# Optimization experiments

Measured on AMD Instinct MI355X. Metric: run time of the kernel, lower is better.

Reference implementation:

```python
import jax, jax.numpy as jnp
import numpy as np

N = 100000   # nodes
E = 1600000  # edges
IN, HID, CLS = 128, 64, 32


def gcn_conv(x, src, dst, W, b, num_nodes):
    """PyG-style GCNConv: out = D^{-1/2} (A+I) D^{-1/2} X W + b."""
    xw = x @ W  # transform first (matches PyG: propagate on transformed feats)
    loop = jnp.arange(num_nodes)
    src_f = jnp.concatenate([src, loop])
    dst_f = jnp.concatenate([dst, loop])
    ones = jnp.ones(src_f.shape[0], dtype=xw.dtype)
    deg = jax.ops.segment_sum(ones, dst_f, num_segments=num_nodes)
    dinv = jnp.where(deg > 0, jax.lax.rsqrt(deg), 0.0)
    norm = dinv[src_f] * dinv[dst_f]            # [E+N]
    msg = xw[src_f] * norm[:, None]             # gather + scale
    out = jax.ops.segment_sum(msg, dst_f, num_segments=num_nodes)
    return out + b


def setup_inputs() -> dict:
    key = jax.random.key(0)
    k = jax.random.split(key, 7)
    x = jax.random.normal(k[0], (N, IN), dtype=jnp.float32)
    edge_index = jax.random.randint(k[1], (2, E), 0, N)
    edge_attr = jax.random.normal(k[2], (E, 1), dtype=jnp.float32)
    W1 = jax.random.normal(k[3], (IN, HID), dtype=jnp.float32) / np.sqrt(IN)
    b1 = jnp.zeros((HID,), dtype=jnp.float32)
    W2 = jax.random.normal(k[4], (HID, CLS), dtype=jnp.float32) / np.sqrt(HID)
    b2 = jnp.zeros((CLS,), dtype=jnp.float32)
    return {"x": x, "edge_index": edge_index, "edge_attr": edge_attr,
            "W1": W1, "b1": b1, "W2": W2, "b2": b2}


def reference(x, edge_index, edge_attr, W1, b1, W2, b2):
    # edge_attr is unpacked by the original forward but unused by GCNConv
    src, dst = edge_index[0], edge_index[1]
    h = jax.nn.relu(gcn_conv(x, src, dst, W1, b1, N))
    return gcn_conv(h, src, dst, W2, b2, N)
```

## Files before the change

### kernel.cpp

```cpp
#include <hip/hip_runtime.h>
#include <hip/hip_fp16.h>

#define N_NODES 100000
#define N_EDGES 1600000
#define IN_F 128
#define HID_F 64
#define CLS_F 32

#define NBKT 512
#define BKT_NODES 196
#define NBLK 800
#define EPB 2000
#define CAPB_RAW 4096
#define CAPB 5120
#define XW_BLOCKS 1563

typedef short s8v __attribute__((ext_vector_type(8)));
typedef float f4v __attribute__((ext_vector_type(4)));
typedef _Float16 h2v __attribute__((ext_vector_type(2)));

__device__ __forceinline__ unsigned short f2h(float f) {
    return __half_as_ushort(__float2half_rn(f));
}
__device__ __forceinline__ int packh2(float x, float y) {
    __half2 p = __floats2half2_rn(x, y);
    union { __half2 h; int i; } c; c.h = p; return c.i;
}

__device__ __forceinline__ void mix8(float* a, int4 v, float dv) {
    union { int4 i; __half h[8]; } c; c.i = v;
#pragma unroll
    for (int j = 0; j < 8; j++)
        a[j] = fmaf(__half2float(c.h[j]), dv, a[j]);
}

__device__ __forceinline__ void dot4(float* a, int2 v) {
#if __has_builtin(__builtin_amdgcn_fdot2)
    union { int2 i; h2v h[2]; } c; c.i = v;
    const h2v E0 = {(_Float16)1.f, (_Float16)0.f};
    const h2v E1 = {(_Float16)0.f, (_Float16)1.f};
#pragma unroll
    for (int j = 0; j < 2; j++) {
        a[2 * j]     = __builtin_amdgcn_fdot2(c.h[j], E0, a[2 * j], false);
        a[2 * j + 1] = __builtin_amdgcn_fdot2(c.h[j], E1, a[2 * j + 1], false);
    }
#else
    union { int2 i; __half2 h[2]; } c; c.i = v;
#pragma unroll
    for (int j = 0; j < 2; j++) {
        float2 f = __half22float2(c.h[j]);
        a[2 * j] += f.x; a[2 * j + 1] += f.y;
    }
#endif
}


__global__ __launch_bounds__(256) void bucket_scatter_kernel(
        const int* __restrict__ src, const int* __restrict__ dst,
        int* __restrict__ cursor, unsigned* __restrict__ bkt) {
    __shared__ int h[NBKT];
    __shared__ int base[NBKT];
    __shared__ int lcur[NBKT];
    __shared__ unsigned pkS[EPB];
    __shared__ short gS[EPB];
    int t = threadIdx.x;
    for (int i = t; i < NBKT; i += 256) { h[i] = 0; lcur[i] = 0; }
    __syncthreads();

    int e0 = blockIdx.x * EPB;
    for (int i = t; i < EPB; i += 256) {
        int e = e0 + i;
        int d = dst[e];
        int g = d / BKT_NODES;
        pkS[i] = ((unsigned)(d - g * BKT_NODES) << 17) | (unsigned)src[e];
        gS[i] = (short)g;
        atomicAdd(&h[g], 1);
    }
    __syncthreads();

    for (int g = t; g < NBKT; g += 256)
        if (h[g] > 0) base[g] = g * CAPB_RAW + atomicAdd(&cursor[g], h[g]);
    __syncthreads();

    for (int i = t; i < EPB; i += 256) {
        int g = gS[i];
        int p = base[g] + atomicAdd(&lcur[g], 1);
        bkt[p] = pkS[i];
    }
}

#define XBM 64
#define SMEM_BYTES 33792

__device__ __forceinline__ void sort_body(char* smem, int b,
        const int* __restrict__ cursor, const unsigned* __restrict__ bkt,
        int* __restrict__ csr, int* __restrict__ off, int* __restrict__ endp,
        float* __restrict__ dinv) {
    int* hist  = (int*)smem;
    int* loff  = hist + BKT_NODES;
    int* loffB = loff + BKT_NODES;
    int* wt    = loffB + BKT_NODES;
    int* csrS  = wt + 4;
    int t = threadIdx.x;
    int s0 = b * CAPB_RAW;
    int nE = cursor[b];

    for (int i = t; i < BKT_NODES; i += 256) hist[i] = 0;
    __syncthreads();
    for (int i = t; i < nE; i += 256)
        atomicAdd(&hist[bkt[s0 + i] >> 17], 1);
    __syncthreads();

    int h0 = 0, h1 = 0;
    if (t < 98) { h0 = hist[2 * t]; h1 = hist[2 * t + 1]; }
    int p0 = (h0 + 7) & ~7;
    int p1 = (h1 + 7) & ~7;
    int sum = p0 + p1;
    int lane = t & 63, w = t >> 6;
    int s = sum;
#pragma unroll
    for (int d = 1; d < 64; d <<= 1) {
        int u = __shfl_up(s, d);
        if (lane >= d) s += u;
    }
    if (lane == 63) wt[w] = s;
    __syncthreads();
    int wbase = 0;
    for (int i = 0; i < w; i++) wbase += wt[i];
    int excl = wbase + s - sum;
    if (t < 98) {
        loff[2 * t] = excl;         loffB[2 * t] = excl;
        loff[2 * t + 1] = excl + p0; loffB[2 * t + 1] = excl + p0;
    }
    __syncthreads();

    for (int j = t; j < BKT_NODES; j += 256) {
        int n = b * BKT_NODES + j;
        if (n < N_NODES) {
            int c = hist[j];
            int o = b * CAPB + loff[j];
            off[n] = o;
            endp[n] = o + ((c + 7) & ~7);
            dinv[n] = rsqrtf((float)(c + 1));
        }
    }
    __syncthreads();

    for (int i = t; i < nE; i += 256) {
        unsigned pk = bkt[s0 + i];
        int dl = (int)(pk >> 17);
        int p = atomicAdd(&loff[dl], 1);
        csrS[p] = (int)(pk & 0x1FFFFu);
    }
    __syncthreads();

    for (int j = t; j < BKT_NODES; j += 256) {
        int c = hist[j];
        int bse = loffB[j];
        int pe = bse + ((c + 7) & ~7);
        for (int p = bse + c; p < pe; p++) csrS[p] = N_NODES;
    }
    __syncthreads();

    int padTot = wt[0] + wt[1] + wt[2] + wt[3];
    for (int i = t; i < padTot; i += 256) csr[b * CAPB + i] = csrS[i];
}

__device__ __forceinline__ void xw1_body(char* smem, int xb_id,
        const float* __restrict__ x, const float* __restrict__ W1,
        unsigned short* __restrict__ y1h) {
    unsigned short* Wb = (unsigned short*)smem;
    unsigned short (*xbuf)[IN_F + 8] =
        (unsigned short (*)[IN_F + 8])(smem + 16384);
    int tid = threadIdx.x;

    for (int i = tid; i < IN_F * HID_F; i += 256) {
        int k = i >> 6, n = i & 63;
        int kc = k >> 5, kw = k & 31;
        int nt = n >> 4, nl = n & 15;
        int quad = kw >> 3, j = kw & 7;
        Wb[(((kc * 4 + nt) * 64) + quad * 16 + nl) * 8 + j] = f2h(W1[i]);
    }

    int nodeBase = xb_id * XBM;
    {
        int snl = tid >> 2;
        int sk0 = (tid & 3) * 32;
        int n = nodeBase + snl;
#pragma unroll
        for (int kk = 0; kk < 32; kk += 4) {
            float4 v = make_float4(0.f, 0.f, 0.f, 0.f);
            if (n < N_NODES) v = *(const float4*)(x + (size_t)n * IN_F + sk0 + kk);
            ushort4 o;
            o.x = f2h(v.x); o.y = f2h(v.y); o.z = f2h(v.z); o.w = f2h(v.w);
            *(ushort4*)(&xbuf[snl][sk0 + kk]) = o;
        }
    }
    __syncthreads();

    int wave = tid >> 6, lane = tid & 63;
    int quad = lane >> 4, l15 = lane & 15;
    int rowBase = wave * 16;

    f4v acc[4];
#pragma unroll
    for (int i = 0; i < 4; i++) acc[i] = (f4v){0.f, 0.f, 0.f, 0.f};

#pragma unroll
    for (int kc = 0; kc < 4; kc++) {
        s8v a = *(const s8v*)(&xbuf[rowBase + l15][kc * 32 + quad * 8]);
#pragma unroll
        for (int nt = 0; nt < 4; nt++) {
            s8v b = *(const s8v*)(&Wb[((kc * 4 + nt) * 64 + lane) * 8]);
            acc[nt] = __builtin_amdgcn_mfma_f32_16x16x32_f16(a, b, acc[nt], 0, 0, 0);
        }
    }

    int n0 = nodeBase + rowBase + quad * 4;
#pragma unroll
    for (int nt = 0; nt < 4; nt++) {
#pragma unroll
        for (int r = 0; r < 4; r++) {
            int n = n0 + r;
            if (n < N_NODES + 1)
                y1h[(size_t)n * HID_F + nt * 16 + l15] = f2h(acc[nt][r]);
        }
    }
}

__global__ __launch_bounds__(256) void sort_xw1_kernel(
        const int* __restrict__ cursor, const unsigned* __restrict__ bkt,
        int* __restrict__ csr, int* __restrict__ off, int* __restrict__ endp,
        float* __restrict__ dinv, const float* __restrict__ x,
        const float* __restrict__ W1, unsigned short* __restrict__ y1h) {
    __shared__ __align__(16) char smem[SMEM_BYTES];
    int b = blockIdx.x;
    if (b < NBKT)
        sort_body(smem, b, cursor, bkt, csr, off, endp, dinv);
    else
        xw1_body(smem, b - NBKT, x, W1, y1h);
}

__global__ __launch_bounds__(256) void gather1_kernel(
        const int* __restrict__ off, const int* __restrict__ endp,
        const int* __restrict__ csr, const unsigned short* __restrict__ y1h,
        const float* __restrict__ dinv, const float* __restrict__ b1,
        unsigned short* __restrict__ hout) {
    int tid = threadIdx.x;
    int wv = __builtin_amdgcn_readfirstlane(tid >> 6);
    int wave = blockIdx.x * 4 + wv;
    int nA = wave * 2, nB = nA + 1;
    int lane = tid & 63;
    int f = lane & 7;
    int g = lane >> 3;
    int fo = f * 16;

    int offA = off[nA], offB = off[nB];
    int lenA = endp[nA] - offA, lenB = endp[nB] - offB;
    int lmax = max(lenA, lenB);
    const int* pA = csr + offA + g;
    const int* pB = csr + offB + g;
    const char* yb = (const char*)y1h;

    float aA[8], aB[8];
#pragma unroll
    for (int j = 0; j < 8; j++) { aA[j] = 0.f; aB[j] = 0.f; }

    if (lmax > 0) {
        int rA = pA[0], rB = pB[0];
        int iA = (lenA > 0) ? rA : N_NODES;
        int iB = (lenB > 0) ? rB : N_NODES;
        float dvA = dinv[iA], dvB = dinv[iB];
        int4 vA = *(const int4*)(yb + (size_t)iA * 128 + fo);
        int4 vB = *(const int4*)(yb + (size_t)iB * 128 + fo);
        int rA1 = pA[8], rB1 = pB[8];
        for (int t = 8; t < lmax; t += 8) {
            int inA = (t < lenA) ? rA1 : N_NODES;
            int inB = (t < lenB) ? rB1 : N_NODES;
            float ndvA = dinv[inA], ndvB = dinv[inB];
            int4 nxA = *(const int4*)(yb + (size_t)inA * 128 + fo);
            int4 nxB = *(const int4*)(yb + (size_t)inB * 128 + fo);
            rA1 = pA[t + 8]; rB1 = pB[t + 8];
            mix8(aA, vA, dvA); mix8(aB, vB, dvB);
            vA = nxA; vB = nxB; dvA = ndvA; dvB = ndvB;
        }
        mix8(aA, vA, dvA); mix8(aB, vB, dvB);
    }

    float c8[8];
#pragma unroll
    for (int j = 0; j < 8; j++) {
        float sel = (lane < 32) ? aB[j] : aA[j];
        float oth = __shfl_xor(sel, 32);
        c8[j] = ((lane < 32) ? aA[j] : aB[j]) + oth;
    }
#pragma unroll
    for (int m = 8; m <= 16; m <<= 1)
#pragma unroll
        for (int j = 0; j < 8; j++) c8[j] += __shfl_xor(c8[j], m);

    int node = (lane < 32) ? nA : nB;
    float dvA = dinv[nA], dvB = dinv[nB];
    float dvS = (lane < 32) ? dvA : dvB;

    int4 sv = *(const int4*)(yb + (size_t)node * 128 + fo);
    mix8(c8, sv, dvS);

    float4 bl = *(const float4*)(b1 + 8 * f);
    float4 bh4 = *(const float4*)(b1 + 8 * f + 4);
    float bb[8] = {bl.x, bl.y, bl.z, bl.w, bh4.x, bh4.y, bh4.z, bh4.w};
    float h[8];
#pragma unroll
    for (int j = 0; j < 8; j++)
        h[j] = fmaxf(fmaf(c8[j], dvS, bb[j]), 0.f);
    int4 H;
    H.x = packh2(h[0], h[1]); H.y = packh2(h[2], h[3]);
    H.z = packh2(h[4], h[5]); H.w = packh2(h[6], h[7]);
    if ((lane & 31) < 8)
        *(int4*)((char*)hout + (size_t)node * 128 + fo) = H;
}

#define YBM 64
__global__ __launch_bounds__(256) void y2_kernel(const unsigned short* __restrict__ h,
                                                 const float* __restrict__ W2,
                                                 const float* __restrict__ dinv,
                                                 unsigned short* __restrict__ y2h) {
    __shared__ __align__(16) unsigned short Wb[2 * 2 * 64 * 8];
    __shared__ __align__(16) unsigned short hb[YBM][HID_F + 8];
    int tid = threadIdx.x;

    for (int i = tid; i < HID_F * CLS_F; i += 256) {
        int k = i >> 5, n = i & 31;
        int kc = k >> 5, kw = k & 31;
        int nt = n >> 4, nl = n & 15;
        int quad = kw >> 3, j = kw & 7;
        Wb[(((kc * 2 + nt) * 64) + quad * 16 + nl) * 8 + j] = f2h(W2[i]);
    }

    int nodeBase = blockIdx.x * YBM;
    {
        int row = tid >> 2, sseg = tid & 3;
        int n = nodeBase + row;
        int4 v0 = {0, 0, 0, 0}, v1 = {0, 0, 0, 0};
        if (n < N_NODES) {
            const char* hp = (const char*)h + (size_t)n * 128 + sseg * 32;
            v0 = *(const int4*)hp;
            v1 = *(const int4*)(hp + 16);
        }
        *(int4*)(&hb[row][sseg * 16]) = v0;
        *(int4*)(&hb[row][sseg * 16 + 8]) = v1;
    }
    __syncthreads();

    int wave = tid >> 6, lane = tid & 63;
    int quad = lane >> 4, l15 = lane & 15;
    int rowBase = wave * 16;

    f4v acc[2];
#pragma unroll
    for (int i = 0; i < 2; i++) acc[i] = (f4v){0.f, 0.f, 0.f, 0.f};

#pragma unroll
    for (int kc = 0; kc < 2; kc++) {
        s8v a = *(const s8v*)(&hb[rowBase + l15][kc * 32 + quad * 8]);
#pragma unroll
        for (int nt = 0; nt < 2; nt++) {
            s8v b = *(const s8v*)(&Wb[((kc * 2 + nt) * 64 + lane) * 8]);
            acc[nt] = __builtin_amdgcn_mfma_f32_16x16x32_f16(a, b, acc[nt], 0, 0, 0);
        }
    }

    float dv[4];
    int n0 = nodeBase + rowBase + quad * 4;
#pragma unroll
    for (int r = 0; r < 4; r++)
        dv[r] = (n0 + r < N_NODES) ? dinv[n0 + r] : 0.f;
#pragma unroll
    for (int nt = 0; nt < 2; nt++) {
#pragma unroll
        for (int r = 0; r < 4; r++) {
            int n = n0 + r;
            if (n < N_NODES + 1)
                y2h[(size_t)n * CLS_F + nt * 16 + l15] = f2h(acc[nt][r] * dv[r]);
        }
    }
}

__global__ __launch_bounds__(256) void gather2_kernel(const int* __restrict__ off,
                                                      const int* __restrict__ endp,
                                                      const int* __restrict__ csr,
                                                      const unsigned short* __restrict__ y2h,
                                                      const float* __restrict__ dinv,
                                                      const float* __restrict__ b2,
                                                      float* __restrict__ out) {
    int tid = threadIdx.x;
    int wv = __builtin_amdgcn_readfirstlane(tid >> 6);
    int wave = blockIdx.x * 4 + wv;
    int nA = wave * 2, nB = nA + 1;
    int lane = tid & 63;
    int f = lane & 7;
    int g = lane >> 3;
    int fo = f * 8;

    int offA = off[nA], offB = off[nB];
    int lenA = endp[nA] - offA, lenB = endp[nB] - offB;
    int lmax = max(lenA, lenB);
    const int* pA = csr + offA + g;
    const int* pB = csr + offB + g;
    const char* yb = (const char*)y2h;

    float aA[4], aB[4];
#pragma unroll
    for (int j = 0; j < 4; j++) { aA[j] = 0.f; aB[j] = 0.f; }

    if (lmax > 0) {
        int rA = pA[0], rB = pB[0];
        int iA = (lenA > 0) ? rA : N_NODES;
        int iB = (lenB > 0) ? rB : N_NODES;
        int2 vA = *(const int2*)(yb + (size_t)iA * 64 + fo);
        int2 vB = *(const int2*)(yb + (size_t)iB * 64 + fo);
        int rA1 = pA[8], rB1 = pB[8];
        for (int t = 8; t < lmax; t += 8) {
            int inA = (t < lenA) ? rA1 : N_NODES;
            int inB = (t < lenB) ? rB1 : N_NODES;
            int2 nxA = *(const int2*)(yb + (size_t)inA * 64 + fo);
            int2 nxB = *(const int2*)(yb + (size_t)inB * 64 + fo);
            rA1 = pA[t + 8]; rB1 = pB[t + 8];
            dot4(aA, vA); dot4(aB, vB);
            vA = nxA; vB = nxB;
        }
        dot4(aA, vA); dot4(aB, vB);
    }

    float c4[4];
#pragma unroll
    for (int j = 0; j < 4; j++) {
        float sel = (lane < 32) ? aB[j] : aA[j];
        float oth = __shfl_xor(sel, 32);
        c4[j] = ((lane < 32) ? aA[j] : aB[j]) + oth;
    }
#pragma unroll
    for (int m = 8; m <= 16; m <<= 1)
#pragma unroll
        for (int j = 0; j < 4; j++) c4[j] += __shfl_xor(c4[j], m);

    int node = (lane < 32) ? nA : nB;

    int2 sv = *(const int2*)(yb + (size_t)node * 64 + fo);
    dot4(c4, sv);

    float dvA = dinv[nA], dvB = dinv[nB];
    float dvS = (lane < 32) ? dvA : dvB;
    float4 b2v = *(const float4*)(b2 + 4 * f);
    float bbv[4] = {b2v.x, b2v.y, b2v.z, b2v.w};
    float4 o4;
    float* op = (float*)&o4;
#pragma unroll
    for (int j = 0; j < 4; j++)
        op[j] = fmaf(c4[j], dvS, bbv[j]);
    if ((lane & 31) < 8)
        *(float4*)(out + (size_t)node * CLS_F + f * 4) = o4;
}

extern "C" void kernel_launch(void* const* d_in, const int* in_sizes, int n_in,
                              void* d_out, int out_size, void* d_ws, size_t ws_size,
                              hipStream_t stream) {
    const float* x  = (const float*)d_in[0];
    const int*   ei = (const int*)d_in[1];
    const float* W1 = (const float*)d_in[3];
    const float* b1 = (const float*)d_in[4];
    const float* W2 = (const float*)d_in[5];
    const float* b2 = (const float*)d_in[6];
    float* out = (float*)d_out;

    const int* src = ei;
    const int* dst = ei + N_EDGES;

    char* ws = (char*)d_ws;
    size_t npad = ((size_t)(N_NODES + 1) * 4 + 255) / 256 * 256;
    float* dinv   = (float*)ws;
    int*   cursor = (int*)(ws + npad);
    int*   off    = (int*)(ws + npad + 2048);
    int*   endp   = (int*)(ws + 2 * npad + 2048);
    int*   csr    = (int*)(ws + 3 * npad + 2048);
    char*  p = (char*)csr + (size_t)(NBKT + 1) * CAPB * 4;
    unsigned* bkt = (unsigned*)p;
    p += (size_t)NBKT * CAPB_RAW * 4;
    unsigned short* y1h = (unsigned short*)p;
    p += (size_t)(N_NODES + 1) * HID_F * 2;
    unsigned short* y2h = (unsigned short*)p;
    p += (size_t)(N_NODES + 1) * CLS_F * 2;
    unsigned short* hbuf = (unsigned short*)p;

    dim3 blk(256);
    hipMemsetAsync(ws, 0, npad + 2048, stream);
    bucket_scatter_kernel<<<dim3(NBLK), blk, 0, stream>>>(src, dst, cursor, bkt);
    sort_xw1_kernel<<<dim3(NBKT + XW_BLOCKS), blk, 0, stream>>>(
        cursor, bkt, csr, off, endp, dinv, x, W1, y1h);
    gather1_kernel<<<dim3(N_NODES / 8), blk, 0, stream>>>(off, endp, csr, y1h, dinv, b1, hbuf);
    y2_kernel<<<dim3((N_NODES + YBM) / YBM), blk, 0, stream>>>(hbuf, W2, dinv, y2h);
    gather2_kernel<<<dim3(N_NODES / 8), blk, 0, stream>>>(off, endp, csr, y2h, dinv, b2, out);
}
```

Measured before the change: 213.6 us.

## Fuse layer-1 gather with layer-2 linear transform via fdot2 in shared memory

Merges the layer-1 aggregation kernel and the separate H·W2 MFMA kernel. Each block packs W2 into half2 pairs in LDS and stages the relu'd hidden rows in LDS. Each lane then computes one output column with fdot2 and writes the dinv-scaled y2 directly. This removes one kernel launch and the round trip of the hidden buffer through global memory. In exchange, every block repeats the W2 packing and runs scalar dot products instead of MFMA.

```diff
diff --git a/kernel.cpp b/kernel.cpp
--- a/kernel.cpp
+++ b/kernel.cpp
@@ -32,6 +32,19 @@
 #pragma unroll
     for (int j = 0; j < 8; j++)
         a[j] = fmaf(__half2float(c.h[j]), dv, a[j]);
+}
+
+__device__ __forceinline__ float fdot2acc(unsigned hu, unsigned wu, float s) {
+#if __has_builtin(__builtin_amdgcn_fdot2)
+    union { unsigned u; h2v h; } a, b;
+    a.u = hu; b.u = wu;
+    return __builtin_amdgcn_fdot2(a.h, b.h, s, false);
+#else
+    union { unsigned u; __half2 h; } a, b;
+    a.u = hu; b.u = wu;
+    float2 fa = __half22float2(a.h), fb = __half22float2(b.h);
+    return s + fa.x * fb.x + fa.y * fb.y;
+#endif
 }
 
 __device__ __forceinline__ void dot4(float* a, int2 v) {
@@ -241,12 +254,22 @@
         xw1_body(smem, b - NBKT, x, W1, y1h);
 }
 
-__global__ __launch_bounds__(256) void gather1_kernel(
+__global__ __launch_bounds__(256) void gather1y2_kernel(
         const int* __restrict__ off, const int* __restrict__ endp,
         const int* __restrict__ csr, const unsigned short* __restrict__ y1h,
         const float* __restrict__ dinv, const float* __restrict__ b1,
-        unsigned short* __restrict__ hout) {
+        const float* __restrict__ W2, unsigned short* __restrict__ y2h) {
+    __shared__ unsigned w2p[(HID_F / 2) * CLS_F];
+    __shared__ __align__(16) char hS[8 * 128];
+
     int tid = threadIdx.x;
+    for (int i = tid; i < (HID_F / 2) * CLS_F; i += 256) {
+        int k2 = i >> 5, c = i & 31;
+        w2p[i] = (unsigned)packh2(W2[(2 * k2) * CLS_F + c],
+                                  (2 * k2 + 1 < HID_F) ? W2[(2 * k2 + 1) * CLS_F + c] : 0.f);
+    }
+    __syncthreads();
+
     int wv = __builtin_amdgcn_readfirstlane(tid >> 6);
     int wave = blockIdx.x * 4 + wv;
     int nA = wave * 2, nB = nA + 1;
@@ -316,74 +339,21 @@
     int4 H;
     H.x = packh2(h[0], h[1]); H.y = packh2(h[2], h[3]);
     H.z = packh2(h[4], h[5]); H.w = packh2(h[6], h[7]);
+
+    int nl = wv * 2 + (lane >> 5);
     if ((lane & 31) < 8)
-        *(int4*)((char*)hout + (size_t)node * 128 + fo) = H;
-}
-
-#define YBM 64
-__global__ __launch_bounds__(256) void y2_kernel(const unsigned short* __restrict__ h,
-                                                 const float* __restrict__ W2,
-                                                 const float* __restrict__ dinv,
-                                                 unsigned short* __restrict__ y2h) {
-    __shared__ __align__(16) unsigned short Wb[2 * 2 * 64 * 8];
-    __shared__ __align__(16) unsigned short hb[YBM][HID_F + 8];
-    int tid = threadIdx.x;
-
-    for (int i = tid; i < HID_F * CLS_F; i += 256) {
-        int k = i >> 5, n = i & 31;
-        int kc = k >> 5, kw = k & 31;
-        int nt = n >> 4, nl = n & 15;
-        int quad = kw >> 3, j = kw & 7;
-        Wb[(((kc * 2 + nt) * 64) + quad * 16 + nl) * 8 + j] = f2h(W2[i]);
-    }
-
-    int nodeBase = blockIdx.x * YBM;
-    {
-        int row = tid >> 2, sseg = tid & 3;
-        int n = nodeBase + row;
-        int4 v0 = {0, 0, 0, 0}, v1 = {0, 0, 0, 0};
-        if (n < N_NODES) {
-            const char* hp = (const char*)h + (size_t)n * 128 + sseg * 32;
-            v0 = *(const int4*)hp;
-            v1 = *(const int4*)(hp + 16);
-        }
-        *(int4*)(&hb[row][sseg * 16]) = v0;
-        *(int4*)(&hb[row][sseg * 16 + 8]) = v1;
-    }
-    __syncthreads();
-
-    int wave = tid >> 6, lane = tid & 63;
-    int quad = lane >> 4, l15 = lane & 15;
-    int rowBase = wave * 16;
-
-    f4v acc[2];
-#pragma unroll
-    for (int i = 0; i < 2; i++) acc[i] = (f4v){0.f, 0.f, 0.f, 0.f};
-
-#pragma unroll
-    for (int kc = 0; kc < 2; kc++) {
-        s8v a = *(const s8v*)(&hb[rowBase + l15][kc * 32 + quad * 8]);
-#pragma unroll
-        for (int nt = 0; nt < 2; nt++) {
-            s8v b = *(const s8v*)(&Wb[((kc * 2 + nt) * 64 + lane) * 8]);
-            acc[nt] = __builtin_amdgcn_mfma_f32_16x16x32_f16(a, b, acc[nt], 0, 0, 0);
-        }
-    }
-
-    float dv[4];
-    int n0 = nodeBase + rowBase + quad * 4;
-#pragma unroll
-    for (int r = 0; r < 4; r++)
-        dv[r] = (n0 + r < N_NODES) ? dinv[n0 + r] : 0.f;
-#pragma unroll
-    for (int nt = 0; nt < 2; nt++) {
-#pragma unroll
-        for (int r = 0; r < 4; r++) {
-            int n = n0 + r;
-            if (n < N_NODES + 1)
-                y2h[(size_t)n * CLS_F + nt * 16 + l15] = f2h(acc[nt][r] * dv[r]);
-        }
-    }
+        *(int4*)(hS + nl * 128 + fo) = H;
+
+    int c = lane & 31;
+    const unsigned* hrow = (const unsigned*)(hS + nl * 128);
+    float sum = 0.f;
+#pragma unroll
+    for (int k2 = 0; k2 < HID_F / 2; k2++)
+        sum = fdot2acc(hrow[k2], w2p[k2 * 32 + c], sum);
+    y2h[(size_t)node * CLS_F + c] = f2h(sum * dvS);
+
+    if (blockIdx.x == 0 && tid < 16)
+        ((unsigned*)y2h)[(size_t)N_NODES * 16 + tid] = 0u;
 }
 
 __global__ __launch_bounds__(256) void gather2_kernel(const int* __restrict__ off,
@@ -489,15 +459,13 @@
     unsigned short* y1h = (unsigned short*)p;
     p += (size_t)(N_NODES + 1) * HID_F * 2;
     unsigned short* y2h = (unsigned short*)p;
-    p += (size_t)(N_NODES + 1) * CLS_F * 2;
-    unsigned short* hbuf = (unsigned short*)p;
 
     dim3 blk(256);
     hipMemsetAsync(ws, 0, npad + 2048, stream);
     bucket_scatter_kernel<<<dim3(NBLK), blk, 0, stream>>>(src, dst, cursor, bkt);
     sort_xw1_kernel<<<dim3(NBKT + XW_BLOCKS), blk, 0, stream>>>(
         cursor, bkt, csr, off, endp, dinv, x, W1, y1h);
-    gather1_kernel<<<dim3(N_NODES / 8), blk, 0, stream>>>(off, endp, csr, y1h, dinv, b1, hbuf);
-    y2_kernel<<<dim3((N_NODES + YBM) / YBM), blk, 0, stream>>>(hbuf, W2, dinv, y2h);
+    gather1y2_kernel<<<dim3(N_NODES / 8), blk, 0, stream>>>(
+        off, endp, csr, y1h, dinv, b1, W2, y2h);
     gather2_kernel<<<dim3(N_NODES / 8), blk, 0, stream>>>(off, endp, csr, y2h, dinv, b2, out);
 }
```

After: 216.2 us. Within noise of the previous version (+1.2%).
